# Kernel tuning notes

Measured on AMD Instinct MI355X. Metric: run time of the kernel, lower is better.

## Reference

```python
import jax, jax.numpy as jnp
import numpy as np

B, C_IN, H, W = 1, 3, 96, 96
NB_CLASSES = 21
NB_ITER = 5
THETA_ALPHA, THETA_BETA, THETA_GAMMA = 160.0, 3.0, 3.0


def setup_inputs() -> dict:
    key = jax.random.key(0)
    ks = jax.random.split(key, 8)
    image = jax.random.uniform(ks[0], (B, C_IN, H, W), jnp.float32)
    net_w = jax.random.normal(ks[1], (NB_CLASSES, C_IN, 3, 3), jnp.float32) * 0.1
    net_b = jax.random.normal(ks[2], (NB_CLASSES,), jnp.float32) * 0.01
    sp_w = jax.random.normal(ks[3], (NB_CLASSES, NB_CLASSES), jnp.float32) * 0.1
    sp_b = jnp.zeros((NB_CLASSES,), jnp.float32)
    bl_w = jax.random.normal(ks[4], (NB_CLASSES, NB_CLASSES), jnp.float32) * 0.1
    bl_b = jnp.zeros((NB_CLASSES,), jnp.float32)
    comp_w = jax.random.normal(ks[5], (NB_CLASSES, NB_CLASSES), jnp.float32) * 0.1
    comp_b = jnp.zeros((NB_CLASSES,), jnp.float32)
    return {"image": image, "net_w": net_w, "net_b": net_b,
            "sp_w": sp_w, "sp_b": sp_b, "bl_w": bl_w, "bl_b": bl_b,
            "comp_w": comp_w, "comp_b": comp_b}


def _gauss_kernel(feat):
    # feat: [B, N, D] -> K[B, N, N] = exp(-||f_i - f_j||^2 / 2)
    sq = jnp.sum(feat * feat, axis=-1)
    d2 = sq[:, :, None] + sq[:, None, :] - 2.0 * jnp.einsum('bnd,bmd->bnm', feat, feat)
    return jnp.exp(-0.5 * jnp.maximum(d2, 0.0))


def _crf_forward(image, net_w, net_b, sp_w, sp_b, bl_w, bl_b, comp_w, comp_b):
    b, c_in, h, w = image.shape
    n = h * w
    nb_classes = net_w.shape[0]
    # unary network: 3x3 same conv
    unaries = jax.lax.conv_general_dilated(
        image, net_w, (1, 1), 'SAME',
        dimension_numbers=('NCHW', 'OIHW', 'NCHW')) + net_b[None, :, None, None]
    # feature-space Gaussian kernels (exact form the permutohedral lattice approximates)
    yy, xx = jnp.meshgrid(jnp.arange(h, dtype=jnp.float32),
                          jnp.arange(w, dtype=jnp.float32), indexing='ij')
    pos = jnp.stack([xx.ravel(), yy.ravel()], axis=-1)          # [N, 2]
    pos_b = jnp.broadcast_to(pos, (b, n, 2))
    img_flat = image.reshape(b, c_in, n).transpose(0, 2, 1)      # [B, N, Cin]
    k_sp = _gauss_kernel(pos_b / THETA_GAMMA)                    # spatial kernel
    k_bl = _gauss_kernel(jnp.concatenate(
        [pos_b / THETA_ALPHA, img_flat / THETA_BETA], axis=-1))  # bilateral kernel
    norm_sp = k_sp.sum(-1)                                       # [B, N]
    norm_bl = k_bl.sum(-1)

    def filt(k, norm, s):
        return jnp.einsum('bnm,bcm->bcn', k, s) / norm[:, None, :]

    u = unaries.reshape(b, nb_classes, n)
    q = u
    s = jax.nn.softmax(q, axis=1)
    for _ in range(NB_ITER):
        sp = filt(k_sp, norm_sp, s)
        bl = filt(k_bl, norm_bl, s)
        mp = (jnp.einsum('oc,bcn->bon', sp_w, sp) + sp_b[None, :, None]
              + jnp.einsum('oc,bcn->bon', bl_w, bl) + bl_b[None, :, None])
        pairwise = jnp.einsum('oc,bcn->bon', comp_w, mp) + comp_b[None, :, None]
        q = u - pairwise
        s = jax.nn.softmax(q, axis=1)
    return s.reshape(b, nb_classes, h, w)


def reference(image, net_w, net_b, sp_w, sp_b, bl_w, bl_b, comp_w, comp_b):
    return _crf_forward(image, net_w, net_b, sp_w, sp_b, bl_w, bl_b, comp_w, comp_b)
```

## Files before the change

### kernel.cpp

```cpp
#include <hip/hip_runtime.h>

#define NPIX 9216
#define IMH 96
#define IMW 96
#define NC 21
#define NCH 22
#define CP 24
#define NMON 126
#define RAD 15
#define NITER 5
#define MG 11
#define NMG 12
#define LDSS 260
#define MPAD 2816

__constant__ float GW[16] = {
    1.0f, 0.945959f, 0.800737f, 0.606531f, 0.411112f, 0.249352f,
    0.135335f, 0.0657285f, 0.0285655f, 0.0111090f, 0.00386592f,
    0.00120386f, 0.000335463f, 8.36523e-05f, 1.86640e-05f, 3.72665e-06f};

__constant__ float d_bk[5] = {1.000000f, 0.998959f, 0.509936f, 0.139441f, 0.070024f};

__global__ __launch_bounds__(64) void p1_kernel(
    const float* __restrict__ img, const float* __restrict__ net_w,
    const float* __restrict__ net_b,
    float* __restrict__ u_pm, float* __restrict__ f_pm, float* __restrict__ M0)
{
    __shared__ float wsh[28];
    const int bid = blockIdx.x, tid = threadIdx.x;
    if (bid < 21 * 144) {
        const int c = bid / 144, chunk = bid % 144;
        if (tid < 27) wsh[tid] = net_w[c * 27 + tid];
        if (tid == 28) wsh[27] = net_b[c];
        __syncthreads();
        const int px = chunk * 64 + tid;
        const int i = px / IMW, j = px % IMW;
        float acc = wsh[27];
        for (int ci = 0; ci < 3; ci++)
            for (int ky = 0; ky < 3; ky++)
                for (int kx = 0; kx < 3; kx++) {
                    const int ii = i + ky - 1, jj = j + kx - 1;
                    float v = 0.f;
                    if (ii >= 0 && ii < IMH && jj >= 0 && jj < IMW)
                        v = img[(ci * IMH + ii) * IMW + jj];
                    acc = fmaf(v, wsh[(ci * 3 + ky) * 3 + kx], acc);
                }
        u_pm[px * CP + c] = acc;
    } else {
        const int chunk = bid - 21 * 144;
        const int px = chunk * 64 + tid;
        if (px < 2772) M0[px] = 0.f;
        const int i = px / IMW, j = px % IMW;
        const float f1 = (float)j * (1.0f / 160.0f);
        const float f2 = (float)i * (1.0f / 160.0f);
        const float f3 = img[0 * NPIX + px] * (1.0f / 3.0f);
        const float f4 = img[1 * NPIX + px] * (1.0f / 3.0f);
        const float f5 = img[2 * NPIX + px] * (1.0f / 3.0f);
        const float env = __expf(-0.5f * (f1*f1 + f2*f2 + f3*f3 + f4*f4 + f5*f5));
        float4* fp = (float4*)(f_pm + px * 8);
        fp[0] = make_float4(f1, f2, f3, f4);
        fp[1] = make_float4(f5, env, 0.f, 0.f);
    }
}

__global__ __launch_bounds__(64) void p2_kernel(
    const float* __restrict__ u_pm, const float* __restrict__ f_pm,
    float* __restrict__ s_pm, float* __restrict__ s_cm, float* __restrict__ phi)
{
    const int bid = blockIdx.x, tid = threadIdx.x;
    if (bid < 144) {
        const int px = bid * 64 + tid;
        float a[NC];
        const float4* up = (const float4*)(u_pm + px * CP);
        #pragma unroll
        for (int v = 0; v < 5; v++) {
            const float4 t = up[v];
            a[4*v] = t.x; a[4*v+1] = t.y; a[4*v+2] = t.z; a[4*v+3] = t.w;
        }
        a[20] = u_pm[px * CP + 20];
        float mx = a[0];
        #pragma unroll
        for (int o = 1; o < NC; o++) mx = fmaxf(mx, a[o]);
        float sum = 0.f;
        #pragma unroll
        for (int o = 0; o < NC; o++) { a[o] = __expf(a[o] - mx); sum += a[o]; }
        const float inv = 1.f / sum;
        #pragma unroll
        for (int o = 0; o < NC; o++) a[o] *= inv;
        float4* sp = (float4*)(s_pm + px * CP);
        sp[0] = make_float4(a[0], a[1], a[2], a[3]);
        sp[1] = make_float4(a[4], a[5], a[6], a[7]);
        sp[2] = make_float4(a[8], a[9], a[10], a[11]);
        sp[3] = make_float4(a[12], a[13], a[14], a[15]);
        sp[4] = make_float4(a[16], a[17], a[18], a[19]);
        sp[5] = make_float4(a[20], 1.f, 0.f, 0.f);
        #pragma unroll
        for (int o = 0; o < NC; o++) s_cm[(size_t)o * NPIX + px] = a[o];
        s_cm[(size_t)21 * NPIX + px] = 1.f;
    } else {
        const int t2 = bid - 144;
        const int m = t2 >> 2, quad = t2 & 3;
        int e1 = 0, e2 = 0, e3 = 0, e4 = 0, e5 = 0, cnt = 0;
        bool done = false;
        for (int a = 0; a <= 4 && !done; a++)
            for (int b2 = 0; b2 <= 4 - a && !done; b2++)
                for (int c = 0; c <= 4 - a - b2 && !done; c++)
                    for (int d = 0; d <= 4 - a - b2 - c && !done; d++) {
                        const int rem = 4 - a - b2 - c - d;
                        if (m - cnt <= rem) {
                            e1 = a; e2 = b2; e3 = c; e4 = d; e5 = m - cnt; done = true;
                        } else cnt += rem + 1;
                    }
        const float fact[5] = {1.f, 1.f, 2.f, 6.f, 24.f};
        const int k = e1 + e2 + e3 + e4 + e5;
        const float sg = sqrtf(d_bk[k] * fact[k] /
                               (fact[e1] * fact[e2] * fact[e3] * fact[e4] * fact[e5]));
        for (int kk = 0; kk < 36; kk++) {
            const int px = quad * 2304 + kk * 64 + tid;
            const float4 fa = *(const float4*)(f_pm + px * 8);
            const float4 fb = *(const float4*)(f_pm + px * 8 + 4);
            float p = fb.y * sg;
            for (int q = 0; q < e1; q++) p *= fa.x;
            for (int q = 0; q < e2; q++) p *= fa.y;
            for (int q = 0; q < e3; q++) p *= fa.z;
            for (int q = 0; q < e4; q++) p *= fa.w;
            for (int q = 0; q < e5; q++) p *= fb.x;
            phi[(size_t)m * NPIX + px] = p;
        }
    }
}

__global__ __launch_bounds__(256) void k1_kernel(
    const float* __restrict__ s_pm, const float* __restrict__ s_cm,
    const float* __restrict__ phi, float* __restrict__ sx, float* __restrict__ M)
{
    __shared__ float smem[(NCH + MG) * LDSS];
    const int bid = blockIdx.x, tid = threadIdx.x;
    if (bid < NMG * 36) {
        const int g = bid / 36, chunk = bid % 36;
        const int m0 = g * MG;
        const int mcnt = (NMON - m0 < MG) ? (NMON - m0) : MG;
        float* s_sh = smem;
        float* p_sh = smem + NCH * LDSS;
        {
            const float4* sp = (const float4*)(s_pm + (size_t)(chunk * 256 + tid) * CP);
            #pragma unroll
            for (int v = 0; v < 6; v++) {
                const float4 t = sp[v];
                const int c = 4 * v;
                if (c < NCH)     s_sh[c * LDSS + tid] = t.x;
                if (c + 1 < NCH) s_sh[(c + 1) * LDSS + tid] = t.y;
                if (c + 2 < NCH) s_sh[(c + 2) * LDSS + tid] = t.z;
                if (c + 3 < NCH) s_sh[(c + 3) * LDSS + tid] = t.w;
            }
        }
        for (int idx = tid; idx < mcnt * 64; idx += 256) {
            const int mm = idx >> 6, p4 = idx & 63;
            const float4 t = *(const float4*)(phi + (size_t)(m0 + mm) * NPIX +
                                              chunk * 256 + p4 * 4);
            *(float4*)(p_sh + mm * LDSS + p4 * 4) = t;
        }
        __syncthreads();
        const int c = tid % NCH, msub = tid / NCH;
        if (msub < mcnt) {
            const float* sr = s_sh + c * LDSS;
            const float* pr = p_sh + msub * LDSS;
            float acc = 0.f;
            for (int p4 = 0; p4 < 64; p4++) {
                const float4 sv = *(const float4*)(sr + p4 * 4);
                const float4 pv = *(const float4*)(pr + p4 * 4);
                acc += pv.x * sv.x + pv.y * sv.y + pv.z * sv.z + pv.w * sv.w;
            }
            atomicAdd(&M[(m0 + msub) * NCH + c], acc);
        }
    } else {
        const int u2 = bid - NMG * 36;
        const int ch = u2 / 36, pc = u2 % 36;
        const int n = pc * 256 + tid, j = n % IMW;
        const float* row = s_cm + (size_t)ch * NPIX + (n - j);
        float a = GW[0] * row[j];
        #pragma unroll
        for (int d = 1; d <= RAD; d++) {
            const float l = (j - d >= 0) ? row[j - d] : 0.f;
            const float r = (j + d < IMW) ? row[j + d] : 0.f;
            a = fmaf(GW[d], l + r, a);
        }
        sx[(size_t)ch * NPIX + n] = a;
    }
}

__global__ __launch_bounds__(256) void k2_kernel(
    const float* __restrict__ sx, const float* __restrict__ phi,
    const float* __restrict__ M, float* __restrict__ Mnext,
    const float* __restrict__ u_pm,
    const float* __restrict__ sp_w, const float* __restrict__ sp_b,
    const float* __restrict__ bl_w, const float* __restrict__ bl_b,
    const float* __restrict__ comp_w, const float* __restrict__ comp_b,
    float* __restrict__ s_pm, float* __restrict__ s_cm,
    float* __restrict__ out, int write_out)
{
    __shared__ float phi_sh[NMON * 64];
    __shared__ float Msh[NMON * CP];
    __shared__ float cy_sh[64 * 25];
    __shared__ float blv_sh[64 * 25];
    __shared__ float wsh[1449];
    const int tid = threadIdx.x;
    const int px0 = blockIdx.x * 64;

    for (int i = tid; i < NMON * CP; i += 256) {
        const int mm = i / CP, c = i % CP;
        Msh[i] = (c < NCH) ? M[mm * NCH + c] : 0.f;
    }
    for (int i = tid; i < 441; i += 256) {
        wsh[i] = sp_w[i]; wsh[441 + i] = bl_w[i]; wsh[882 + i] = comp_w[i];
    }
    if (tid < 21) {
        wsh[1323 + tid] = sp_b[tid]; wsh[1344 + tid] = bl_b[tid];
        wsh[1365 + tid] = comp_b[tid];
    }
    if (blockIdx.x < 44) {
        const int i = blockIdx.x * 64 + tid;
        if (i < 2772) Mnext[i] = 0.f;
    }

    for (int idx = tid; idx < NMON * 16; idx += 256) {
        const int m = idx >> 4, grp = idx & 15;
        *(float4*)(phi_sh + m * 64 + grp * 4) =
            *(const float4*)(phi + (size_t)m * NPIX + px0 + grp * 4);
    }
    for (int task = tid; task < NCH * 64; task += 256) {
        const int ch = task >> 6, p = task & 63;
        const int n = px0 + p, i = n / IMW;
        const float* plane = sx + (size_t)ch * NPIX;
        float a = GW[0] * plane[n];
        #pragma unroll
        for (int d = 1; d <= RAD; d++) {
            const float t = (i - d >= 0) ? plane[n - d * IMW] : 0.f;
            const float b = (i + d < IMH) ? plane[n + d * IMW] : 0.f;
            a = fmaf(GW[d], t + b, a);
        }
        cy_sh[p * 25 + ch] = a;
    }
    __syncthreads();

    {
        const int cq = tid >> 6, p = tid & 63;
        const int c0 = cq * 6;
        float acc[6] = {0.f, 0.f, 0.f, 0.f, 0.f, 0.f};
        for (int mm = 0; mm < NMON; mm++) {
            const float ph = phi_sh[mm * 64 + p];
            const float* Mr = Msh + mm * CP + c0;
            #pragma unroll
            for (int k = 0; k < 6; k++) acc[k] = fmaf(ph, Mr[k], acc[k]);
        }
        #pragma unroll
        for (int k = 0; k < 6; k++)
            if (c0 + k < NCH) blv_sh[p * 25 + c0 + k] = acc[k];
    }
    __syncthreads();

    if (tid < 64) {
        const int n = px0 + tid;
        float spv[NCH], blv[NCH];
        #pragma unroll
        for (int c = 0; c < NCH; c++) {
            spv[c] = cy_sh[tid * 25 + c];
            blv[c] = blv_sh[tid * 25 + c];
        }
        const float invS = 1.f / spv[21];
        const float invB = 1.f / blv[21];
        #pragma unroll
        for (int c = 0; c < NC; c++) { spv[c] *= invS; blv[c] *= invB; }

        float mp[NC];
        for (int o = 0; o < NC; o++) {
            float m = wsh[1323 + o] + wsh[1344 + o];
            #pragma unroll
            for (int c = 0; c < NC; c++)
                m += wsh[o * NC + c] * spv[c] + wsh[441 + o * NC + c] * blv[c];
            mp[o] = m;
        }
        float q[NC];
        for (int o = 0; o < NC; o++) {
            float m = wsh[1365 + o];
            #pragma unroll
            for (int c = 0; c < NC; c++) m += wsh[882 + o * NC + c] * mp[c];
            q[o] = u_pm[(size_t)n * CP + o] - m;
        }
        float mx = q[0];
        #pragma unroll
        for (int o = 1; o < NC; o++) mx = fmaxf(mx, q[o]);
        float sum = 0.f;
        #pragma unroll
        for (int o = 0; o < NC; o++) { q[o] = __expf(q[o] - mx); sum += q[o]; }
        const float inv = 1.f / sum;
        #pragma unroll
        for (int o = 0; o < NC; o++) q[o] *= inv;

        float4* sp = (float4*)(s_pm + (size_t)n * CP);
        sp[0] = make_float4(q[0], q[1], q[2], q[3]);
        sp[1] = make_float4(q[4], q[5], q[6], q[7]);
        sp[2] = make_float4(q[8], q[9], q[10], q[11]);
        sp[3] = make_float4(q[12], q[13], q[14], q[15]);
        sp[4] = make_float4(q[16], q[17], q[18], q[19]);
        sp[5] = make_float4(q[20], 1.f, 0.f, 0.f);
        #pragma unroll
        for (int o = 0; o < NC; o++) s_cm[(size_t)o * NPIX + n] = q[o];
        s_cm[(size_t)21 * NPIX + n] = 1.f;
        if (write_out)
            #pragma unroll
            for (int o = 0; o < NC; o++) out[(size_t)o * NPIX + n] = q[o];
    }
}

extern "C" void kernel_launch(void* const* d_in, const int* in_sizes, int n_in,
                              void* d_out, int out_size, void* d_ws, size_t ws_size,
                              hipStream_t stream) {
    const float* img    = (const float*)d_in[0];
    const float* net_w  = (const float*)d_in[1];
    const float* net_b  = (const float*)d_in[2];
    const float* sp_w   = (const float*)d_in[3];
    const float* sp_b   = (const float*)d_in[4];
    const float* bl_w   = (const float*)d_in[5];
    const float* bl_b   = (const float*)d_in[6];
    const float* comp_w = (const float*)d_in[7];
    const float* comp_b = (const float*)d_in[8];

    float* u_pm = (float*)d_ws;
    float* s_pm = u_pm + (size_t)NPIX * CP;
    float* s_cm = s_pm + (size_t)NPIX * CP;
    float* f_pm = s_cm + (size_t)NCH * NPIX;
    float* sx   = f_pm + (size_t)NPIX * 8;
    float* phi  = sx + (size_t)NCH * NPIX;
    float* M    = phi + (size_t)NMON * NPIX;

    float* out = (float*)d_out;

    p1_kernel<<<dim3(21 * 144 + 144), dim3(64), 0, stream>>>(
        img, net_w, net_b, u_pm, f_pm, M);
    p2_kernel<<<dim3(144 + NMON * 4), dim3(64), 0, stream>>>(
        u_pm, f_pm, s_pm, s_cm, phi);
    for (int it = 0; it < NITER; it++) {
        float* Mc = M + (it & 1) * MPAD;
        float* Mn = M + ((it + 1) & 1) * MPAD;
        k1_kernel<<<dim3(NMG * 36 + NCH * 36), dim3(256), 0, stream>>>(
            s_pm, s_cm, phi, sx, Mc);
        k2_kernel<<<dim3(144), dim3(256), 0, stream>>>(
            sx, phi, Mc, Mn, u_pm, sp_w, sp_b, bl_w, bl_b, comp_w, comp_b,
            s_pm, s_cm, out, it == NITER - 1 ? 1 : 0);
    }
}
```

Baseline: 243.5 us.

## Fuse prep kernels and split k2 into 32-pixel blocks with parallel matvecs

The two preprocessing kernels (conv, softmax, feature and monomial computation) are merged into a single prep kernel with one thread per pixel. Monomial powers come from a small per-thread power table in shared memory, and the intermediate f_pm buffer is dropped. The per-iteration k2 kernel now uses 32-pixel blocks, doubling the grid. Its compatibility matvecs are spread across all 256 threads through shared memory instead of running on 64 threads. The aim is to remove a launch and to raise parallelism in the serial tail of k2. The cost is more block-level synchronisation, and a prep kernel that runs only 144 small blocks.

```diff
diff --git a/kernel.cpp b/kernel.cpp
--- a/kernel.cpp
+++ b/kernel.cpp
@@ -21,85 +21,20 @@
 
 __constant__ float d_bk[5] = {1.000000f, 0.998959f, 0.509936f, 0.139441f, 0.070024f};
 
-__global__ __launch_bounds__(64) void p1_kernel(
+__global__ __launch_bounds__(64) void prep_kernel(
     const float* __restrict__ img, const float* __restrict__ net_w,
     const float* __restrict__ net_b,
-    float* __restrict__ u_pm, float* __restrict__ f_pm, float* __restrict__ M0)
+    float* __restrict__ u_pm, float* __restrict__ s_pm, float* __restrict__ s_cm,
+    float* __restrict__ phi, float* __restrict__ M0)
 {
-    __shared__ float wsh[28];
-    const int bid = blockIdx.x, tid = threadIdx.x;
-    if (bid < 21 * 144) {
-        const int c = bid / 144, chunk = bid % 144;
-        if (tid < 27) wsh[tid] = net_w[c * 27 + tid];
-        if (tid == 28) wsh[27] = net_b[c];
-        __syncthreads();
-        const int px = chunk * 64 + tid;
-        const int i = px / IMW, j = px % IMW;
-        float acc = wsh[27];
-        for (int ci = 0; ci < 3; ci++)
-            for (int ky = 0; ky < 3; ky++)
-                for (int kx = 0; kx < 3; kx++) {
-                    const int ii = i + ky - 1, jj = j + kx - 1;
-                    float v = 0.f;
-                    if (ii >= 0 && ii < IMH && jj >= 0 && jj < IMW)
-                        v = img[(ci * IMH + ii) * IMW + jj];
-                    acc = fmaf(v, wsh[(ci * 3 + ky) * 3 + kx], acc);
-                }
-        u_pm[px * CP + c] = acc;
-    } else {
-        const int chunk = bid - 21 * 144;
-        const int px = chunk * 64 + tid;
-        if (px < 2772) M0[px] = 0.f;
-        const int i = px / IMW, j = px % IMW;
-        const float f1 = (float)j * (1.0f / 160.0f);
-        const float f2 = (float)i * (1.0f / 160.0f);
-        const float f3 = img[0 * NPIX + px] * (1.0f / 3.0f);
-        const float f4 = img[1 * NPIX + px] * (1.0f / 3.0f);
-        const float f5 = img[2 * NPIX + px] * (1.0f / 3.0f);
-        const float env = __expf(-0.5f * (f1*f1 + f2*f2 + f3*f3 + f4*f4 + f5*f5));
-        float4* fp = (float4*)(f_pm + px * 8);
-        fp[0] = make_float4(f1, f2, f3, f4);
-        fp[1] = make_float4(f5, env, 0.f, 0.f);
-    }
-}
-
-__global__ __launch_bounds__(64) void p2_kernel(
-    const float* __restrict__ u_pm, const float* __restrict__ f_pm,
-    float* __restrict__ s_pm, float* __restrict__ s_cm, float* __restrict__ phi)
-{
-    const int bid = blockIdx.x, tid = threadIdx.x;
-    if (bid < 144) {
-        const int px = bid * 64 + tid;
-        float a[NC];
-        const float4* up = (const float4*)(u_pm + px * CP);
-        #pragma unroll
-        for (int v = 0; v < 5; v++) {
-            const float4 t = up[v];
-            a[4*v] = t.x; a[4*v+1] = t.y; a[4*v+2] = t.z; a[4*v+3] = t.w;
-        }
-        a[20] = u_pm[px * CP + 20];
-        float mx = a[0];
-        #pragma unroll
-        for (int o = 1; o < NC; o++) mx = fmaxf(mx, a[o]);
-        float sum = 0.f;
-        #pragma unroll
-        for (int o = 0; o < NC; o++) { a[o] = __expf(a[o] - mx); sum += a[o]; }
-        const float inv = 1.f / sum;
-        #pragma unroll
-        for (int o = 0; o < NC; o++) a[o] *= inv;
-        float4* sp = (float4*)(s_pm + px * CP);
-        sp[0] = make_float4(a[0], a[1], a[2], a[3]);
-        sp[1] = make_float4(a[4], a[5], a[6], a[7]);
-        sp[2] = make_float4(a[8], a[9], a[10], a[11]);
-        sp[3] = make_float4(a[12], a[13], a[14], a[15]);
-        sp[4] = make_float4(a[16], a[17], a[18], a[19]);
-        sp[5] = make_float4(a[20], 1.f, 0.f, 0.f);
-        #pragma unroll
-        for (int o = 0; o < NC; o++) s_cm[(size_t)o * NPIX + px] = a[o];
-        s_cm[(size_t)21 * NPIX + px] = 1.f;
-    } else {
-        const int t2 = bid - 144;
-        const int m = t2 >> 2, quad = t2 & 3;
+    __shared__ float wsh[567], bsh[21];
+    __shared__ float sg_sh[NMON];
+    __shared__ float ex_sh[NMON * 5];
+    __shared__ float pt[64 * 25];
+    const int tid = threadIdx.x;
+    for (int i = tid; i < 567; i += 64) wsh[i] = net_w[i];
+    if (tid < 21) bsh[tid] = net_b[tid];
+    for (int m = tid; m < NMON; m += 64) {
         int e1 = 0, e2 = 0, e3 = 0, e4 = 0, e5 = 0, cnt = 0;
         bool done = false;
         for (int a = 0; a <= 4 && !done; a++)
@@ -113,20 +48,83 @@
                     }
         const float fact[5] = {1.f, 1.f, 2.f, 6.f, 24.f};
         const int k = e1 + e2 + e3 + e4 + e5;
-        const float sg = sqrtf(d_bk[k] * fact[k] /
-                               (fact[e1] * fact[e2] * fact[e3] * fact[e4] * fact[e5]));
-        for (int kk = 0; kk < 36; kk++) {
-            const int px = quad * 2304 + kk * 64 + tid;
-            const float4 fa = *(const float4*)(f_pm + px * 8);
-            const float4 fb = *(const float4*)(f_pm + px * 8 + 4);
-            float p = fb.y * sg;
-            for (int q = 0; q < e1; q++) p *= fa.x;
-            for (int q = 0; q < e2; q++) p *= fa.y;
-            for (int q = 0; q < e3; q++) p *= fa.z;
-            for (int q = 0; q < e4; q++) p *= fa.w;
-            for (int q = 0; q < e5; q++) p *= fb.x;
-            phi[(size_t)m * NPIX + px] = p;
-        }
+        sg_sh[m] = sqrtf(d_bk[k] * fact[k] /
+                         (fact[e1] * fact[e2] * fact[e3] * fact[e4] * fact[e5]));
+        ex_sh[m * 5 + 0] = (float)e1; ex_sh[m * 5 + 1] = (float)e2;
+        ex_sh[m * 5 + 2] = (float)e3; ex_sh[m * 5 + 3] = (float)e4;
+        ex_sh[m * 5 + 4] = (float)e5;
+    }
+    __syncthreads();
+
+    const int px = blockIdx.x * 64 + tid;
+    const int i = px / IMW, j = px % IMW;
+    if (px < 2772) M0[px] = 0.f;
+
+    float acc[NC];
+    #pragma unroll
+    for (int o = 0; o < NC; o++) acc[o] = bsh[o];
+    for (int ci = 0; ci < 3; ci++)
+        for (int ky = 0; ky < 3; ky++)
+            for (int kx = 0; kx < 3; kx++) {
+                const int ii = i + ky - 1, jj = j + kx - 1;
+                float v = 0.f;
+                if (ii >= 0 && ii < IMH && jj >= 0 && jj < IMW)
+                    v = img[(ci * IMH + ii) * IMW + jj];
+                #pragma unroll
+                for (int o = 0; o < NC; o++)
+                    acc[o] = fmaf(v, wsh[(ci * 3 + ky) * 3 + kx + o * 27], acc[o]);
+            }
+    {
+        float4* up = (float4*)(u_pm + (size_t)px * CP);
+        up[0] = make_float4(acc[0], acc[1], acc[2], acc[3]);
+        up[1] = make_float4(acc[4], acc[5], acc[6], acc[7]);
+        up[2] = make_float4(acc[8], acc[9], acc[10], acc[11]);
+        up[3] = make_float4(acc[12], acc[13], acc[14], acc[15]);
+        up[4] = make_float4(acc[16], acc[17], acc[18], acc[19]);
+        up[5] = make_float4(acc[20], 0.f, 0.f, 0.f);
+    }
+    float mx = acc[0];
+    #pragma unroll
+    for (int o = 1; o < NC; o++) mx = fmaxf(mx, acc[o]);
+    float sum = 0.f;
+    #pragma unroll
+    for (int o = 0; o < NC; o++) { acc[o] = __expf(acc[o] - mx); sum += acc[o]; }
+    const float inv = 1.f / sum;
+    #pragma unroll
+    for (int o = 0; o < NC; o++) acc[o] *= inv;
+    {
+        float4* sp = (float4*)(s_pm + (size_t)px * CP);
+        sp[0] = make_float4(acc[0], acc[1], acc[2], acc[3]);
+        sp[1] = make_float4(acc[4], acc[5], acc[6], acc[7]);
+        sp[2] = make_float4(acc[8], acc[9], acc[10], acc[11]);
+        sp[3] = make_float4(acc[12], acc[13], acc[14], acc[15]);
+        sp[4] = make_float4(acc[16], acc[17], acc[18], acc[19]);
+        sp[5] = make_float4(acc[20], 1.f, 0.f, 0.f);
+    }
+    #pragma unroll
+    for (int o = 0; o < NC; o++) s_cm[(size_t)o * NPIX + px] = acc[o];
+    s_cm[(size_t)21 * NPIX + px] = 1.f;
+
+    const float fv[5] = {(float)j * (1.0f / 160.0f), (float)i * (1.0f / 160.0f),
+                         img[0 * NPIX + px] * (1.0f / 3.0f),
+                         img[1 * NPIX + px] * (1.0f / 3.0f),
+                         img[2 * NPIX + px] * (1.0f / 3.0f)};
+    const float env = __expf(-0.5f * (fv[0]*fv[0] + fv[1]*fv[1] + fv[2]*fv[2] +
+                                      fv[3]*fv[3] + fv[4]*fv[4]));
+    #pragma unroll
+    for (int v = 0; v < 5; v++) {
+        float p = 1.f;
+        #pragma unroll
+        for (int e = 0; e < 5; e++) { pt[tid * 25 + v * 5 + e] = p; p *= fv[v]; }
+    }
+    for (int m = 0; m < NMON; m++) {
+        float p = env * sg_sh[m];
+        p *= pt[tid * 25 + 0 + (int)ex_sh[m * 5 + 0]];
+        p *= pt[tid * 25 + 5 + (int)ex_sh[m * 5 + 1]];
+        p *= pt[tid * 25 + 10 + (int)ex_sh[m * 5 + 2]];
+        p *= pt[tid * 25 + 15 + (int)ex_sh[m * 5 + 3]];
+        p *= pt[tid * 25 + 20 + (int)ex_sh[m * 5 + 4]];
+        phi[(size_t)m * NPIX + px] = p;
     }
 }
 
@@ -199,94 +197,100 @@
     float* __restrict__ s_pm, float* __restrict__ s_cm,
     float* __restrict__ out, int write_out)
 {
-    __shared__ float phi_sh[NMON * 64];
     __shared__ float Msh[NMON * CP];
-    __shared__ float cy_sh[64 * 25];
-    __shared__ float blv_sh[64 * 25];
-    __shared__ float wsh[1449];
+    __shared__ float phi_sh[NMON * 32];
+    __shared__ float cy_sh[32 * 25];
+    __shared__ float blv_sh[32 * 25];
+    __shared__ float mp_sh[32 * CP];
+    __shared__ float q_sh[32 * CP];
+    __shared__ float wsh[1386 + 63];
     const int tid = threadIdx.x;
-    const int px0 = blockIdx.x * 64;
-
-    for (int i = tid; i < NMON * CP; i += 256) {
-        const int mm = i / CP, c = i % CP;
-        Msh[i] = (c < NCH) ? M[mm * NCH + c] : 0.f;
-    }
-    for (int i = tid; i < 441; i += 256) {
-        wsh[i] = sp_w[i]; wsh[441 + i] = bl_w[i]; wsh[882 + i] = comp_w[i];
+    const int px0 = blockIdx.x * 32;
+    const int i0 = px0 / IMW;
+
+    for (int idx = tid; idx < NMON * CP; idx += 256) {
+        const int mm = idx / CP, c = idx % CP;
+        Msh[idx] = (c < NCH) ? M[mm * NCH + c] : 0.f;
+    }
+    for (int idx = tid; idx < 441; idx += 256) {
+        wsh[idx] = sp_w[idx]; wsh[441 + idx] = bl_w[idx]; wsh[882 + idx] = comp_w[idx];
     }
     if (tid < 21) {
         wsh[1323 + tid] = sp_b[tid]; wsh[1344 + tid] = bl_b[tid];
         wsh[1365 + tid] = comp_b[tid];
     }
-    if (blockIdx.x < 44) {
-        const int i = blockIdx.x * 64 + tid;
-        if (i < 2772) Mnext[i] = 0.f;
-    }
-
-    for (int idx = tid; idx < NMON * 16; idx += 256) {
-        const int m = idx >> 4, grp = idx & 15;
-        *(float4*)(phi_sh + m * 64 + grp * 4) =
-            *(const float4*)(phi + (size_t)m * NPIX + px0 + grp * 4);
-    }
-    for (int task = tid; task < NCH * 64; task += 256) {
-        const int ch = task >> 6, p = task & 63;
-        const int n = px0 + p, i = n / IMW;
-        const float* plane = sx + (size_t)ch * NPIX;
-        float a = GW[0] * plane[n];
-        #pragma unroll
-        for (int d = 1; d <= RAD; d++) {
-            const float t = (i - d >= 0) ? plane[n - d * IMW] : 0.f;
-            const float b = (i + d < IMH) ? plane[n + d * IMW] : 0.f;
-            a = fmaf(GW[d], t + b, a);
-        }
-        cy_sh[p * 25 + ch] = a;
+    if (blockIdx.x < 11) {
+        const int idx = blockIdx.x * 256 + tid;
+        if (idx < 2772) Mnext[idx] = 0.f;
+    }
+    for (int idx = tid; idx < NMON * 8; idx += 256) {
+        const int m = idx >> 3, g = idx & 7;
+        *(float4*)(phi_sh + m * 32 + g * 4) =
+            *(const float4*)(phi + (size_t)m * NPIX + px0 + g * 4);
+    }
+    for (int task = tid; task < 24 * 32; task += 256) {
+        const int ch = task >> 5, p = task & 31;
+        if (ch < NCH) {
+            const int n = px0 + p;
+            const float* plane = sx + (size_t)ch * NPIX;
+            float a = GW[0] * plane[n];
+            #pragma unroll
+            for (int d = 1; d <= RAD; d++) {
+                const float t = (i0 - d >= 0) ? plane[n - d * IMW] : 0.f;
+                const float b = (i0 + d < IMH) ? plane[n + d * IMW] : 0.f;
+                a = fmaf(GW[d], t + b, a);
+            }
+            cy_sh[p * 25 + ch] = a;
+        }
     }
     __syncthreads();
 
     {
-        const int cq = tid >> 6, p = tid & 63;
-        const int c0 = cq * 6;
-        float acc[6] = {0.f, 0.f, 0.f, 0.f, 0.f, 0.f};
+        const int p = tid & 31, c0 = (tid >> 5) * 3;
+        float a0 = 0.f, a1 = 0.f, a2 = 0.f;
         for (int mm = 0; mm < NMON; mm++) {
-            const float ph = phi_sh[mm * 64 + p];
+            const float ph = phi_sh[mm * 32 + p];
             const float* Mr = Msh + mm * CP + c0;
-            #pragma unroll
-            for (int k = 0; k < 6; k++) acc[k] = fmaf(ph, Mr[k], acc[k]);
-        }
-        #pragma unroll
-        for (int k = 0; k < 6; k++)
-            if (c0 + k < NCH) blv_sh[p * 25 + c0 + k] = acc[k];
-    }
-    __syncthreads();
-
-    if (tid < 64) {
+            a0 = fmaf(ph, Mr[0], a0);
+            a1 = fmaf(ph, Mr[1], a1);
+            a2 = fmaf(ph, Mr[2], a2);
+        }
+        if (c0 < NCH)     blv_sh[p * 25 + c0] = a0;
+        if (c0 + 1 < NCH) blv_sh[p * 25 + c0 + 1] = a1;
+        if (c0 + 2 < NCH) blv_sh[p * 25 + c0 + 2] = a2;
+    }
+    __syncthreads();
+
+    for (int t = tid; t < 672; t += 256) {
+        const int p = t & 31, o = t >> 5;
+        const float* cyr = cy_sh + p * 25;
+        const float* blr = blv_sh + p * 25;
+        float dS = 0.f, dB = 0.f;
+        #pragma unroll
+        for (int c = 0; c < NC; c++) {
+            dS = fmaf(wsh[o * NC + c], cyr[c], dS);
+            dB = fmaf(wsh[441 + o * NC + c], blr[c], dB);
+        }
+        mp_sh[p * CP + o] = wsh[1323 + o] + wsh[1344 + o] +
+                            dS / cyr[21] + dB / blr[21];
+    }
+    __syncthreads();
+
+    for (int t = tid; t < 672; t += 256) {
+        const int p = t & 31, o = t >> 5;
+        const float* mpr = mp_sh + p * CP;
+        float d = wsh[1365 + o];
+        #pragma unroll
+        for (int c = 0; c < NC; c++) d = fmaf(wsh[882 + o * NC + c], mpr[c], d);
+        q_sh[p * CP + o] = u_pm[(size_t)(px0 + p) * CP + o] - d;
+    }
+    __syncthreads();
+
+    if (tid < 32) {
         const int n = px0 + tid;
-        float spv[NCH], blv[NCH];
-        #pragma unroll
-        for (int c = 0; c < NCH; c++) {
-            spv[c] = cy_sh[tid * 25 + c];
-            blv[c] = blv_sh[tid * 25 + c];
-        }
-        const float invS = 1.f / spv[21];
-        const float invB = 1.f / blv[21];
-        #pragma unroll
-        for (int c = 0; c < NC; c++) { spv[c] *= invS; blv[c] *= invB; }
-
-        float mp[NC];
-        for (int o = 0; o < NC; o++) {
-            float m = wsh[1323 + o] + wsh[1344 + o];
-            #pragma unroll
-            for (int c = 0; c < NC; c++)
-                m += wsh[o * NC + c] * spv[c] + wsh[441 + o * NC + c] * blv[c];
-            mp[o] = m;
-        }
         float q[NC];
-        for (int o = 0; o < NC; o++) {
-            float m = wsh[1365 + o];
-            #pragma unroll
-            for (int c = 0; c < NC; c++) m += wsh[882 + o * NC + c] * mp[c];
-            q[o] = u_pm[(size_t)n * CP + o] - m;
-        }
+        #pragma unroll
+        for (int o = 0; o < NC; o++) q[o] = q_sh[tid * CP + o];
         float mx = q[0];
         #pragma unroll
         for (int o = 1; o < NC; o++) mx = fmaxf(mx, q[o]);
@@ -329,23 +333,20 @@
     float* u_pm = (float*)d_ws;
     float* s_pm = u_pm + (size_t)NPIX * CP;
     float* s_cm = s_pm + (size_t)NPIX * CP;
-    float* f_pm = s_cm + (size_t)NCH * NPIX;
-    float* sx   = f_pm + (size_t)NPIX * 8;
+    float* sx   = s_cm + (size_t)NCH * NPIX;
     float* phi  = sx + (size_t)NCH * NPIX;
     float* M    = phi + (size_t)NMON * NPIX;
 
     float* out = (float*)d_out;
 
-    p1_kernel<<<dim3(21 * 144 + 144), dim3(64), 0, stream>>>(
-        img, net_w, net_b, u_pm, f_pm, M);
-    p2_kernel<<<dim3(144 + NMON * 4), dim3(64), 0, stream>>>(
-        u_pm, f_pm, s_pm, s_cm, phi);
+    prep_kernel<<<dim3(144), dim3(64), 0, stream>>>(
+        img, net_w, net_b, u_pm, s_pm, s_cm, phi, M);
     for (int it = 0; it < NITER; it++) {
         float* Mc = M + (it & 1) * MPAD;
         float* Mn = M + ((it + 1) & 1) * MPAD;
         k1_kernel<<<dim3(NMG * 36 + NCH * 36), dim3(256), 0, stream>>>(
             s_pm, s_cm, phi, sx, Mc);
-        k2_kernel<<<dim3(144), dim3(256), 0, stream>>>(
+        k2_kernel<<<dim3(288), dim3(256), 0, stream>>>(
             sx, phi, Mc, Mn, u_pm, sp_w, sp_b, bl_w, bl_b, comp_w, comp_b,
             s_pm, s_cm, out, it == NITER - 1 ? 1 : 0);
     }
```

Measured after the change: 227.8 us. -6.4%, faster.
